# Kernel optimization log

Hardware: AMD Instinct MI355X
Metric: run time of the kernel (lower is better)

## Reference

```python
import jax, jax.numpy as jnp
import numpy as np

N_SRC, N_DST, N_EDGES = 200000, 100000, 600000
D_IN, D_OUT = 128, 128
NUM_EDGE_TYPES = 7
SCALING_FACTOR = 100.0


def setup_inputs() -> dict:
    key = jax.random.key(0)
    ks = jax.random.split(key, 6)
    x_src = jax.random.normal(ks[0], (N_SRC, D_IN), dtype=jnp.float32)
    x_target = jax.random.normal(ks[1], (N_DST, D_IN), dtype=jnp.float32)
    row = jax.random.randint(ks[2], (N_EDGES,), 0, N_SRC, dtype=jnp.int64 if jax.config.jax_enable_x64 else jnp.int32)
    col = jax.random.randint(ks[3], (N_EDGES,), 0, N_DST, dtype=jnp.int64 if jax.config.jax_enable_x64 else jnp.int32)
    edge_type = jax.random.randint(ks[4], (N_EDGES,), 0, NUM_EDGE_TYPES, dtype=jnp.int32)
    # Parameters (mirroring reset_parameters): xavier_uniform weight, zero bias,
    # relation_weight = 1/scaling_factor constant.
    limit = float(np.sqrt(6.0 / (D_IN + D_OUT)))
    weight = jax.random.uniform(ks[5], (D_IN, D_OUT), minval=-limit, maxval=limit, dtype=jnp.float32)
    bias = jnp.zeros((D_OUT,), dtype=jnp.float32)
    relation_weight = jnp.full((NUM_EDGE_TYPES,), 1.0 / SCALING_FACTOR, dtype=jnp.float32)
    return {"x_src": x_src, "x_target": x_target, "row": row, "col": col,
            "edge_type": edge_type, "weight": weight, "bias": bias,
            "relation_weight": relation_weight}


def reference(x_src, x_target, row, col, edge_type, weight, bias, relation_weight):
    n_dst = x_target.shape[0]
    # per-type linear transform (shared weight, applied to src and target)
    h_src = x_src @ weight                      # [N_src, D_out]
    h_tgt = x_target @ weight                   # [N_dst, D_out] (computed as in original; unused by 'add' aggr)
    # relation weights: one-hot(e_feat) @ leaky_relu(rw * s) == gather
    rw = jax.nn.leaky_relu(relation_weight * SCALING_FACTOR)
    edge_weight = rw[edge_type]                 # [E]
    # weighted in-degree normalization over destination nodes
    deg = jax.ops.segment_sum(edge_weight, col, num_segments=n_dst)  # [N_dst]
    ew = edge_weight / deg[col]                 # [E]
    # gather -> scale -> scatter-add message passing
    msg = ew[:, None] * h_src[row]              # [E, D_out]
    out = jnp.zeros((n_dst, h_src.shape[1]), dtype=h_src.dtype).at[col].add(msg)
    return out + bias
```

## Files before the change

kernel.cpp:

```cpp
#include <hip/hip_runtime.h>

#define D 128
#define CAP 64

typedef __attribute__((ext_vector_type(8))) short bf16x8;
typedef __attribute__((ext_vector_type(4))) float f32x4;
typedef __attribute__((ext_vector_type(8))) ushort ushort8;

struct EW { int r; float w; };

__device__ __forceinline__ float rel_w(const float* __restrict__ rel, int t) {
    float v = rel[t] * 100.0f;
    return v > 0.0f ? v : 0.01f * v;
}

__device__ __forceinline__ ushort f2b(float x) {
    unsigned u = __float_as_uint(x);
    u += 0x7FFFu + ((u >> 16) & 1u);
    return (ushort)(u >> 16);
}

__global__ void k_place(const int* __restrict__ col, const int* __restrict__ row,
                        const int* __restrict__ et, const float* __restrict__ rel,
                        int* __restrict__ cnt, EW* __restrict__ ewr,
                        const float* __restrict__ W, ushort* __restrict__ Wt, int ne) {
    const int e = blockIdx.x * blockDim.x + threadIdx.x;
    if (e < ne) {
        const int c = col[e];
        const int p = atomicAdd(&cnt[c], 1);
        if (p < CAP) {
            EW rec; rec.r = row[e]; rec.w = rel_w(rel, et[e]);
            ewr[(size_t)c * CAP + p] = rec;
        }
    }
    if (e < D * D) {
        const int n = e >> 7, k = e & 127;
        Wt[e] = f2b(W[k * D + n]);
    }
}

__global__ __launch_bounds__(256) void k_agg(const float* __restrict__ X,
                                             const EW* __restrict__ ewr,
                                             const int* __restrict__ cnt,
                                             ushort* __restrict__ Ab, int ndst) {
    const int dw = (int)((blockIdx.x * blockDim.x + threadIdx.x) >> 6);
    const int lane = threadIdx.x & 63;
    if (dw >= ndst) return;
    const int c = min(cnt[dw], CAP);
    const int m16 = lane & 15, g4 = lane >> 4;

    EW e0; e0.r = 0; e0.w = 0.f;
    if (lane < c) e0 = ewr[(size_t)dw * CAP + lane];

    float wsum = e0.w;
    #pragma unroll
    for (int s = 1; s < 64; s <<= 1) wsum += __shfl_xor(wsum, s);
    const float inv = (wsum != 0.f) ? 1.f / wsum : 0.f;

    const int r0 = e0.r; const float wv = e0.w * inv;
    float acc[8] = {};
    {
        int   rr = __shfl(r0, g4);
        float ww = __shfl(wv, g4);
        float4 h0 = *(const float4*)&X[(size_t)rr * D + m16 * 8];
        float4 h1 = *(const float4*)&X[(size_t)rr * D + m16 * 8 + 4];
        for (int j0 = 4; j0 < c; j0 += 4) {
            const int jn = j0 + g4;
            const int   rrn = __shfl(r0, jn);
            const float wwn = __shfl(wv, jn);
            const float4 g0 = *(const float4*)&X[(size_t)rrn * D + m16 * 8];
            const float4 g1 = *(const float4*)&X[(size_t)rrn * D + m16 * 8 + 4];
            acc[0] = fmaf(ww, h0.x, acc[0]); acc[1] = fmaf(ww, h0.y, acc[1]);
            acc[2] = fmaf(ww, h0.z, acc[2]); acc[3] = fmaf(ww, h0.w, acc[3]);
            acc[4] = fmaf(ww, h1.x, acc[4]); acc[5] = fmaf(ww, h1.y, acc[5]);
            acc[6] = fmaf(ww, h1.z, acc[6]); acc[7] = fmaf(ww, h1.w, acc[7]);
            h0 = g0; h1 = g1; ww = wwn;
        }
        acc[0] = fmaf(ww, h0.x, acc[0]); acc[1] = fmaf(ww, h0.y, acc[1]);
        acc[2] = fmaf(ww, h0.z, acc[2]); acc[3] = fmaf(ww, h0.w, acc[3]);
        acc[4] = fmaf(ww, h1.x, acc[4]); acc[5] = fmaf(ww, h1.y, acc[5]);
        acc[6] = fmaf(ww, h1.z, acc[6]); acc[7] = fmaf(ww, h1.w, acc[7]);
    }

    #pragma unroll
    for (int i = 0; i < 8; ++i) {
        acc[i] += __shfl_xor(acc[i], 16);
        acc[i] += __shfl_xor(acc[i], 32);
    }

    if (lane < 16) {
        ushort8 o;
        #pragma unroll
        for (int i = 0; i < 8; ++i) o[i] = f2b(acc[i]);
        *(ushort8*)&Ab[(size_t)dw * D + m16 * 8] = o;
    }
}

__global__ __launch_bounds__(256) void k_mm(const ushort* __restrict__ Ab,
                                            const ushort* __restrict__ Wt,
                                            const float* __restrict__ bias,
                                            float* __restrict__ out, int ndst) {
    __shared__ ushort sW[D * 136];
    __shared__ ushort sA[64 * 136];
    const int t = threadIdx.x;
    const int rbase = blockIdx.x * 64;

    #pragma unroll
    for (int p = 0; p < 8; ++p) {
        const int idx = p * 2048 + t * 8;
        const int n = idx >> 7, k = idx & 127;
        *(bf16x8*)&sW[n * 136 + k] = *(const bf16x8*)&Wt[idx];
    }
    #pragma unroll
    for (int p = 0; p < 4; ++p) {
        const int idx = p * 2048 + t * 8;
        const int r = idx >> 7, k = idx & 127;
        const int gr = rbase + r;
        bf16x8 v = {};
        if (gr < ndst) v = *(const bf16x8*)&Ab[(size_t)gr * D + k];
        *(bf16x8*)&sA[r * 136 + k] = v;
    }
    __syncthreads();

    const int w = t >> 6, l = t & 63;
    const int m16 = l & 15, g4 = l >> 4;
    const int arow = w * 16 + m16;

    f32x4 acc[8] = {};
    #pragma unroll
    for (int ks = 0; ks < 4; ++ks) {
        const int k0 = ks * 32 + g4 * 8;
        const bf16x8 a = *(const bf16x8*)&sA[arow * 136 + k0];
        #pragma unroll
        for (int nf = 0; nf < 8; ++nf) {
            const bf16x8 b = *(const bf16x8*)&sW[(nf * 16 + m16) * 136 + k0];
            acc[nf] = __builtin_amdgcn_mfma_f32_16x16x32_bf16(a, b, acc[nf], 0, 0, 0);
        }
    }

    #pragma unroll
    for (int nf = 0; nf < 8; ++nf) {
        const int colj = nf * 16 + m16;
        const float bv = bias[colj];
        #pragma unroll
        for (int q = 0; q < 4; ++q) {
            const int r = rbase + w * 16 + g4 * 4 + q;
            if (r < ndst) out[(size_t)r * D + colj] = acc[nf][q] + bv;
        }
    }
}

extern "C" void kernel_launch(void* const* d_in, const int* in_sizes, int n_in,
                              void* d_out, int out_size, void* d_ws, size_t ws_size,
                              hipStream_t stream) {
    const float* x_src  = (const float*)d_in[0];
    const int*   row    = (const int*)d_in[2];
    const int*   col    = (const int*)d_in[3];
    const int*   etype  = (const int*)d_in[4];
    const float* weight = (const float*)d_in[5];
    const float* bias   = (const float*)d_in[6];
    const float* relw   = (const float*)d_in[7];

    const int ndst = out_size / D;
    const int ne   = in_sizes[2];

    ushort* Ab  = (ushort*)d_ws;
    ushort* Wt  = Ab + (size_t)ndst * D;
    EW*     ewr = (EW*)(Wt + D * D);
    int*    cnt = (int*)(ewr + (size_t)ndst * CAP);

    float* out = (float*)d_out;

    hipMemsetAsync(cnt, 0, (size_t)ndst * sizeof(int), stream);
    hipLaunchKernelGGL(k_place, dim3((ne + 255) / 256), dim3(256), 0, stream,
                       col, row, etype, relw, cnt, ewr, weight, Wt, ne);
    hipLaunchKernelGGL(k_agg, dim3((ndst + 3) / 4), dim3(256), 0, stream,
                       x_src, ewr, cnt, Ab, ndst);
    hipLaunchKernelGGL(k_mm, dim3((ndst + 63) / 64), dim3(256), 0, stream,
                       Ab, Wt, bias, out, ndst);
}
```

Measured before the change: 111.4 us.

## Reorder to transform sources first, then aggregate bf16 features per destination

Swaps the order of operations so the dense transform is applied to all source rows first, producing a bf16 copy of transformed source features. Aggregation then gathers these half-width rows per destination and writes fp32 output with the bias fused in. This halves the bytes per gathered row, but the GEMM now runs over twice as many rows (all sources, not destinations) and adds a full read of x_src plus a bf16 intermediate write. The edge loop also loses its explicit software prefetch.

```diff
diff --git a/kernel.cpp b/kernel.cpp
--- a/kernel.cpp
+++ b/kernel.cpp
@@ -20,6 +20,10 @@
     return (ushort)(u >> 16);
 }
 
+__device__ __forceinline__ float b2f(ushort u) {
+    return __uint_as_float((unsigned)u << 16);
+}
+
 __global__ void k_place(const int* __restrict__ col, const int* __restrict__ row,
                         const int* __restrict__ et, const float* __restrict__ rel,
                         int* __restrict__ cnt, EW* __restrict__ ewr,
@@ -39,67 +43,9 @@
     }
 }
 
-__global__ __launch_bounds__(256) void k_agg(const float* __restrict__ X,
-                                             const EW* __restrict__ ewr,
-                                             const int* __restrict__ cnt,
-                                             ushort* __restrict__ Ab, int ndst) {
-    const int dw = (int)((blockIdx.x * blockDim.x + threadIdx.x) >> 6);
-    const int lane = threadIdx.x & 63;
-    if (dw >= ndst) return;
-    const int c = min(cnt[dw], CAP);
-    const int m16 = lane & 15, g4 = lane >> 4;
-
-    EW e0; e0.r = 0; e0.w = 0.f;
-    if (lane < c) e0 = ewr[(size_t)dw * CAP + lane];
-
-    float wsum = e0.w;
-    #pragma unroll
-    for (int s = 1; s < 64; s <<= 1) wsum += __shfl_xor(wsum, s);
-    const float inv = (wsum != 0.f) ? 1.f / wsum : 0.f;
-
-    const int r0 = e0.r; const float wv = e0.w * inv;
-    float acc[8] = {};
-    {
-        int   rr = __shfl(r0, g4);
-        float ww = __shfl(wv, g4);
-        float4 h0 = *(const float4*)&X[(size_t)rr * D + m16 * 8];
-        float4 h1 = *(const float4*)&X[(size_t)rr * D + m16 * 8 + 4];
-        for (int j0 = 4; j0 < c; j0 += 4) {
-            const int jn = j0 + g4;
-            const int   rrn = __shfl(r0, jn);
-            const float wwn = __shfl(wv, jn);
-            const float4 g0 = *(const float4*)&X[(size_t)rrn * D + m16 * 8];
-            const float4 g1 = *(const float4*)&X[(size_t)rrn * D + m16 * 8 + 4];
-            acc[0] = fmaf(ww, h0.x, acc[0]); acc[1] = fmaf(ww, h0.y, acc[1]);
-            acc[2] = fmaf(ww, h0.z, acc[2]); acc[3] = fmaf(ww, h0.w, acc[3]);
-            acc[4] = fmaf(ww, h1.x, acc[4]); acc[5] = fmaf(ww, h1.y, acc[5]);
-            acc[6] = fmaf(ww, h1.z, acc[6]); acc[7] = fmaf(ww, h1.w, acc[7]);
-            h0 = g0; h1 = g1; ww = wwn;
-        }
-        acc[0] = fmaf(ww, h0.x, acc[0]); acc[1] = fmaf(ww, h0.y, acc[1]);
-        acc[2] = fmaf(ww, h0.z, acc[2]); acc[3] = fmaf(ww, h0.w, acc[3]);
-        acc[4] = fmaf(ww, h1.x, acc[4]); acc[5] = fmaf(ww, h1.y, acc[5]);
-        acc[6] = fmaf(ww, h1.z, acc[6]); acc[7] = fmaf(ww, h1.w, acc[7]);
-    }
-
-    #pragma unroll
-    for (int i = 0; i < 8; ++i) {
-        acc[i] += __shfl_xor(acc[i], 16);
-        acc[i] += __shfl_xor(acc[i], 32);
-    }
-
-    if (lane < 16) {
-        ushort8 o;
-        #pragma unroll
-        for (int i = 0; i < 8; ++i) o[i] = f2b(acc[i]);
-        *(ushort8*)&Ab[(size_t)dw * D + m16 * 8] = o;
-    }
-}
-
-__global__ __launch_bounds__(256) void k_mm(const ushort* __restrict__ Ab,
-                                            const ushort* __restrict__ Wt,
-                                            const float* __restrict__ bias,
-                                            float* __restrict__ out, int ndst) {
+__global__ __launch_bounds__(256) void k_gemm(const float* __restrict__ X,
+                                              const ushort* __restrict__ Wt,
+                                              ushort* __restrict__ Hb, int nrows) {
     __shared__ ushort sW[D * 136];
     __shared__ ushort sA[64 * 136];
     const int t = threadIdx.x;
@@ -116,9 +62,14 @@
         const int idx = p * 2048 + t * 8;
         const int r = idx >> 7, k = idx & 127;
         const int gr = rbase + r;
-        bf16x8 v = {};
-        if (gr < ndst) v = *(const bf16x8*)&Ab[(size_t)gr * D + k];
-        *(bf16x8*)&sA[r * 136 + k] = v;
+        ushort8 v = {};
+        if (gr < nrows) {
+            const float4 xa = *(const float4*)&X[(size_t)gr * D + k];
+            const float4 xb = *(const float4*)&X[(size_t)gr * D + k + 4];
+            v[0] = f2b(xa.x); v[1] = f2b(xa.y); v[2] = f2b(xa.z); v[3] = f2b(xa.w);
+            v[4] = f2b(xb.x); v[5] = f2b(xb.y); v[6] = f2b(xb.z); v[7] = f2b(xb.w);
+        }
+        *(ushort8*)&sA[r * 136 + k] = v;
     }
     __syncthreads();
 
@@ -141,12 +92,61 @@
     #pragma unroll
     for (int nf = 0; nf < 8; ++nf) {
         const int colj = nf * 16 + m16;
-        const float bv = bias[colj];
         #pragma unroll
         for (int q = 0; q < 4; ++q) {
             const int r = rbase + w * 16 + g4 * 4 + q;
-            if (r < ndst) out[(size_t)r * D + colj] = acc[nf][q] + bv;
+            if (r < nrows) Hb[(size_t)r * D + colj] = f2b(acc[nf][q]);
         }
+    }
+}
+
+__global__ __launch_bounds__(256) void k_agg(const ushort* __restrict__ Hb,
+                                             const EW* __restrict__ ewr,
+                                             const int* __restrict__ cnt,
+                                             const float* __restrict__ bias,
+                                             float* __restrict__ out, int ndst) {
+    const int dw = (int)((blockIdx.x * blockDim.x + threadIdx.x) >> 6);
+    const int lane = threadIdx.x & 63;
+    if (dw >= ndst) return;
+    const int c = min(cnt[dw], CAP);
+    const int m16 = lane & 15, g4 = lane >> 4;
+
+    EW e0; e0.r = 0; e0.w = 0.f;
+    if (lane < c) e0 = ewr[(size_t)dw * CAP + lane];
+
+    float wsum = e0.w;
+    #pragma unroll
+    for (int s = 1; s < 64; s <<= 1) wsum += __shfl_xor(wsum, s);
+    const float inv = (wsum != 0.f) ? 1.f / wsum : 0.f;
+
+    const int r0 = e0.r; const float wv = e0.w * inv;
+    float acc[8] = {};
+    for (int j0 = 0; j0 < c; j0 += 4) {
+        const int j = j0 + g4;
+        const int   rr = __shfl(r0, j);
+        const float ww = __shfl(wv, j);
+        const ushort8 hv = *(const ushort8*)&Hb[(size_t)rr * D + m16 * 8];
+        #pragma unroll
+        for (int i = 0; i < 8; ++i)
+            acc[i] = fmaf(ww, b2f(hv[i]), acc[i]);
+    }
+
+    #pragma unroll
+    for (int i = 0; i < 8; ++i) {
+        acc[i] += __shfl_xor(acc[i], 16);
+        acc[i] += __shfl_xor(acc[i], 32);
+    }
+
+    if (lane < 16) {
+        const float4 b0 = *(const float4*)&bias[m16 * 8];
+        const float4 b1 = *(const float4*)&bias[m16 * 8 + 4];
+        float4 o0, o1;
+        o0.x = acc[0] + b0.x; o0.y = acc[1] + b0.y;
+        o0.z = acc[2] + b0.z; o0.w = acc[3] + b0.w;
+        o1.x = acc[4] + b1.x; o1.y = acc[5] + b1.y;
+        o1.z = acc[6] + b1.z; o1.w = acc[7] + b1.w;
+        *(float4*)&out[(size_t)dw * D + m16 * 8]     = o0;
+        *(float4*)&out[(size_t)dw * D + m16 * 8 + 4] = o1;
     }
 }
 
@@ -161,11 +161,12 @@
     const float* bias   = (const float*)d_in[6];
     const float* relw   = (const float*)d_in[7];
 
+    const int nsrc = in_sizes[0] / D;
     const int ndst = out_size / D;
     const int ne   = in_sizes[2];
 
-    ushort* Ab  = (ushort*)d_ws;
-    ushort* Wt  = Ab + (size_t)ndst * D;
+    ushort* Hb  = (ushort*)d_ws;
+    ushort* Wt  = Hb + (size_t)nsrc * D;
     EW*     ewr = (EW*)(Wt + D * D);
     int*    cnt = (int*)(ewr + (size_t)ndst * CAP);
 
@@ -174,8 +175,8 @@
     hipMemsetAsync(cnt, 0, (size_t)ndst * sizeof(int), stream);
     hipLaunchKernelGGL(k_place, dim3((ne + 255) / 256), dim3(256), 0, stream,
                        col, row, etype, relw, cnt, ewr, weight, Wt, ne);
+    hipLaunchKernelGGL(k_gemm, dim3((nsrc + 63) / 64), dim3(256), 0, stream,
+                       x_src, Wt, Hb, nsrc);
     hipLaunchKernelGGL(k_agg, dim3((ndst + 3) / 4), dim3(256), 0, stream,
-                       x_src, ewr, cnt, Ab, ndst);
-    hipLaunchKernelGGL(k_mm, dim3((ndst + 63) / 64), dim3(256), 0, stream,
-                       Ab, Wt, bias, out, ndst);
+                       Hb, ewr, cnt, bias, out, ndst);
 }
```

New measurement: 111.1 us. No clear change (-0.3%).
